# Optimization experiments

Hardware: AMD Instinct MI355X
Metric: run time of the kernel (lower is better)

The kernel has to match this reference:

```python
import jax, jax.numpy as jnp
import numpy as np

B, T, I, H, C, S, V = 32, 64, 300, 168, 168, 512, 50257


def setup_inputs() -> dict:
    key = jax.random.key(0)
    ks = jax.random.split(key, 10)
    s = 0.05
    return {
        "x": jax.random.normal(ks[0], (B, T, I), jnp.float32),
        "context": jax.random.normal(ks[1], (B, S, C), jnp.float32),
        "context_lengths": jax.random.randint(ks[2], (B,), 1, S + 1),
        "W_ih": jax.random.normal(ks[3], (4 * H, I + C), jnp.float32) * s,
        "W_hh": jax.random.normal(ks[4], (4 * H, H), jnp.float32) * s,
        "b_ih": jnp.zeros((4 * H,), jnp.float32),
        "b_hh": jnp.zeros((4 * H,), jnp.float32),
        "att_Wx": jax.random.normal(ks[5], (H, H), jnp.float32) * s,
        "att_Ws": jax.random.normal(ks[6], (C, H), jnp.float32) * s,
        "att_b": jnp.zeros((H,), jnp.float32),
        "att_v": jax.random.normal(ks[7], (H,), jnp.float32) * s,
        "W_dec": jax.random.normal(ks[8], (V, H), jnp.float32) * s,
    }


def reference(x, context, context_lengths, W_ih, W_hh, b_ih, b_hh,
              att_Wx, att_Ws, att_b, att_v, W_dec):
    # x: (B, T, I); context: (B, S, C)
    b, t, _ = x.shape
    s_len = context.shape[1]
    h_dim = W_hh.shape[1]
    dtype = x.dtype

    # valid-position mask for attention over source context
    mask = jnp.arange(s_len)[None, :] < context_lengths[:, None]  # (B, S)
    # seq projection is time-invariant: precompute once outside the step loop
    seq_proj = jnp.einsum('bsc,ca->bsa', context, att_Ws)  # (B, S, H)

    h0 = jnp.zeros((b, h_dim), dtype)
    c0 = jnp.zeros((b, h_dim), dtype)

    def step(carry, x_t):
        h, c = carry
        # MLP (additive) attention: v . tanh(Wx h + Ws seq + b)
        e = jnp.einsum('bsa,a->bs',
                       jnp.tanh((h @ att_Wx)[:, None, :] + seq_proj + att_b),
                       att_v)  # (B, S)
        e = jnp.where(mask, e, jnp.asarray(-1e9, dtype))
        w = jax.nn.softmax(e, axis=-1)
        attn_ctx = jnp.einsum('bs,bsc->bc', w, context)  # (B, C)

        # concat input with attended context, single-layer LSTM cell
        rnn_in = jnp.concatenate([x_t, attn_ctx], axis=1)  # (B, I+C)
        gates = rnn_in @ W_ih.T + b_ih + h @ W_hh.T + b_hh  # (B, 4H)
        i_g, f_g, g_g, o_g = jnp.split(gates, 4, axis=1)    # torch ifgo order
        c_new = jax.nn.sigmoid(f_g) * c + jax.nn.sigmoid(i_g) * jnp.tanh(g_g)
        h_new = jax.nn.sigmoid(o_g) * jnp.tanh(c_new)

        dec = h_new @ W_dec.T  # (B, V), bias-free decode
        return (h_new, c_new), dec

    _, decs = jax.lax.scan(step, (h0, c0), jnp.swapaxes(x, 0, 1))  # (T, B, V)
    return jnp.swapaxes(decs, 0, 1)  # (B, T, V)
```

## Files before the change

kernel.cpp:

```cpp
#include <hip/hip_runtime.h>
#include <stdint.h>

#define BB 32
#define TT 64
#define ID 300
#define HH 168
#define SS 512
#define VV 50257
#define G4 672
#define IC 468
#define KP 192
#define NP2 50432
#define NJ 8
#define RPB 21
#define CPB 84
#define KK 336
#define WKP 88
#define EPAD 170
#define SBLK 64
#define LSLOT 192
#define HROW 96
#define LP 72
#define NTN 197
#define NTILES 1576

typedef float f32x4 __attribute__((ext_vector_type(4)));
typedef short bf16x8 __attribute__((ext_vector_type(8)));
typedef unsigned long long u64;

__device__ __forceinline__ float bf2f(unsigned short u) {
  union { unsigned int i; float f; } v; v.i = ((unsigned int)u) << 16; return v.f;
}
__device__ __forceinline__ unsigned short f2bf(float f) {
  union { float f; unsigned int u; } v; v.f = f;
  unsigned int r = v.u + 0x7fffu + ((v.u >> 16) & 1u);
  return (unsigned short)(r >> 16);
}
__device__ __forceinline__ float rcpf(float x) { return __builtin_amdgcn_rcpf(x); }
__device__ __forceinline__ u64 packft(float f, unsigned tag) {
  union { float f; unsigned u; } v; v.f = f;
  return ((u64)tag << 32) | (u64)v.u;
}
__device__ __forceinline__ float lo_f(u64 x) {
  union { unsigned u; float f; } v; v.u = (unsigned)x; return v.f;
}
__device__ __forceinline__ unsigned hi_u(u64 x) { return (unsigned)(x >> 32); }
__device__ __forceinline__ void postv(u64* p, u64 v) {
  __hip_atomic_store(p, v, __ATOMIC_RELAXED, __HIP_MEMORY_SCOPE_AGENT);
}
__device__ __forceinline__ u64 loadv(const u64* p) {
  return __hip_atomic_load(p, __ATOMIC_RELAXED, __HIP_MEMORY_SCOPE_AGENT);
}
__device__ __forceinline__ void postu(unsigned* p, unsigned v) {
  __hip_atomic_store(p, v, __ATOMIC_RELAXED, __HIP_MEMORY_SCOPE_AGENT);
}
__device__ __forceinline__ unsigned loadu(const unsigned* p) {
  return __hip_atomic_load(p, __ATOMIC_RELAXED, __HIP_MEMORY_SCOPE_AGENT);
}

#define NB_WDEC 4728
#define NB_TR   788
__global__ void k_prepall(const float* __restrict__ Wih, const float* __restrict__ Whh,
                          const float* __restrict__ attWx, const float* __restrict__ Wd,
                          float* __restrict__ WihxT, unsigned short* __restrict__ Wdb,
                          float* __restrict__ WgT, unsigned short* __restrict__ WxS,
                          u64* __restrict__ Abuf, u64* __restrict__ Pbuf,
                          unsigned* __restrict__ pw) {
  const int bid = blockIdx.x, tid = threadIdx.x;
  if (bid < NB_WDEC) {
    size_t e0 = ((size_t)bid * 256 + tid) * 8;
    int v = (int)(e0 / KP), kp0 = (int)(e0 - (size_t)v * KP);
    int rg = kp0 / 24, off0 = kp0 - rg * 24;
    unsigned short o[8];
    if (v < VV) {
      const float* src = Wd + (size_t)v * HH + rg * RPB + off0;
      #pragma unroll
      for (int i = 0; i < 8; ++i) o[i] = (off0 + i < RPB) ? f2bf(src[i]) : 0;
    } else {
      #pragma unroll
      for (int i = 0; i < 8; ++i) o[i] = 0;
    }
    *(uint4*)(Wdb + e0) = *(const uint4*)o;
    return;
  }
  if (bid < NB_WDEC + NB_TR) {
    int idx = (bid - NB_WDEC) * 256 + tid;
    if (idx < ID * G4) {
      int k = idx / G4, i = idx - k * G4;
      WihxT[idx] = Wih[(size_t)i * IC + k];
    }
    return;
  }
  int idx = (bid - NB_WDEC - NB_TR) * 256 + tid;
  const int T1 = NJ * KK * WKP;
  const int T2 = T1 + NJ * RPB * HH;
  const int ZH = BB * NJ * LSLOT;
  const int T3 = T2 + 2 * ZH + 64;
  if (idx < T1) {
    int j = idx / (KK * WKP); int r = idx - j * (KK * WKP);
    int k = r / WKP, col = r - k * WKP;
    float w = 0.f;
    if (col < CPB) {
      int gt = col / RPB, rr = col - gt * RPB;
      int gcol = gt * HH + j * RPB + rr;
      w = (k < HH) ? Wih[(size_t)gcol * IC + ID + k] : Whh[(size_t)gcol * HH + (k - HH)];
    }
    WgT[idx] = w;
  } else if (idx < T2) {
    int r = idx - T1;
    WxS[r] = f2bf(attWx[r]);
  } else if (idx < T3) {
    int r = idx - T2;
    if (r < ZH) Abuf[r] = 0ull;
    else if (r < 2 * ZH) Pbuf[r - ZH] = 0ull;
    else pw[r - 2 * ZH] = 0u;
  }
}

__global__ void k_seqxp(const float* __restrict__ ctx, const float* __restrict__ Ws,
                        const float* __restrict__ x, const float* __restrict__ WihxT,
                        const float* __restrict__ bih, const float* __restrict__ bhh,
                        unsigned short* __restrict__ ETs, unsigned short* __restrict__ ctxb,
                        float* __restrict__ Xp) {
  __shared__ float sbuf[2688];
  const int tid = threadIdx.x;
  if (blockIdx.x < 1024) {
    const int b = blockIdx.x & 31;
    const int s0 = (blockIdx.x >> 5) * 16;
    for (int idx = tid; idx < 16 * HH; idx += 256) {
      float v = ctx[(size_t)(b * SS + s0) * HH + idx];
      sbuf[idx] = v;
      ctxb[(size_t)(b * SS + s0) * HH + idx] = f2bf(v);
    }
    __syncthreads();
    #pragma unroll
    for (int o = 0; o < 11; ++o) {
      int idx = o * 256 + tid;
      if (idx < 16 * HH) {
        int s = idx / HH, h = idx - s * HH;
        const float* cr = &sbuf[s * HH];
        float acc = 0.f;
        #pragma unroll 4
        for (int c = 0; c < HH; ++c) acc = fmaf(cr[c], Ws[c * HH + h], acc);
        ETs[(size_t)(b * SS + s0 + s) * HH + h] = f2bf(__expf(2.f * acc));
      }
    }
  } else {
    const int r = blockIdx.x - 1024;
    const int t0 = (r & 7) * 8;
    const int b = r >> 3;
    for (int idx = tid; idx < 8 * ID; idx += 256)
      sbuf[idx] = x[(size_t)(b * TT + t0) * ID + idx];
    __syncthreads();
    for (int i = tid; i < G4; i += 256) {
      float bias = bih[i] + bhh[i];
      float acc[8];
      #pragma unroll
      for (int tt = 0; tt < 8; ++tt) acc[tt] = bias;
      for (int k = 0; k < ID; ++k) {
        float w = WihxT[k * G4 + i];
        #pragma unroll
        for (int tt = 0; tt < 8; ++tt) acc[tt] += sbuf[tt * ID + k] * w;
      }
      #pragma unroll
      for (int tt = 0; tt < 8; ++tt)
        Xp[(size_t)(b * TT + t0 + tt) * G4 + i] = acc[tt];
    }
  }
}

__global__ __launch_bounds__(512, 1) void k_recur(
    const int* __restrict__ lens, const float* __restrict__ attb,
    const float* __restrict__ attv, const float* __restrict__ WgT,
    const unsigned short* __restrict__ WxS, const unsigned short* __restrict__ ETs,
    const unsigned short* __restrict__ ctxb, const float* __restrict__ Xp,
    u64* __restrict__ Abuf, u64* __restrict__ Pbuf,
    unsigned* __restrict__ hallA, const unsigned short* __restrict__ Wdb,
    float* __restrict__ out, unsigned* __restrict__ pw) {
  const int b = blockIdx.x & 31;
  const int j = blockIdx.x >> 5;
  const int tid = threadIdx.x;

  __shared__ __align__(16) float WgL[KK][WKP];
  __shared__ unsigned short EL[SBLK][EPAD];
  __shared__ unsigned short WxL[RPB][HH];
  __shared__ float scratch[512];
  __shared__ float redH[504], redC[504];
  __shared__ float gE[HH], hsh[HH], abL[HH], vL[HH], attn[HH];
  __shared__ float esh[SBLK], hLoc[RPB], cLoc[RPB], wsum[8];
  __shared__ float sumv_s, bsum_s;
  __shared__ int sClaim;

  {
    const f32x4* src = (const f32x4*)(WgT + (size_t)j * KK * WKP);
    f32x4* dst = (f32x4*)WgL;
    for (int i = tid; i < KK * WKP / 4; i += 512) dst[i] = src[i];
  }
  for (int i = tid; i < SBLK * HH; i += 512) {
    int s = i / HH, h = i - s * HH;
    EL[s][h] = ETs[((size_t)b * SS + j * SBLK + s) * HH + h];
  }
  for (int i = tid; i < RPB * HH; i += 512)
    ((unsigned short*)WxL)[i] = WxS[(size_t)j * RPB * HH + i];
  if (tid < HH) { abL[tid] = attb[tid]; vL[tid] = attv[tid]; }
  if (tid < RPB) cLoc[tid] = 0.f;
  __syncthreads();
  if (tid == 0) {
    float s = 0.f;
    for (int h = 0; h < HH; ++h) s += vL[h];
    sumv_s = s;
  }
  const int len = lens[b];
  const int sbase = j * SBLK;
  u64* Amine = Abuf + (size_t)(b * NJ + j) * LSLOT;
  u64* Pmine = Pbuf + (size_t)(b * NJ + j) * LSLOT;
  __syncthreads();

  for (int t = 0; t < TT; ++t) {
    float xa0=0,xa1=0,xa2=0,xa3=0, xb0=0,xb1=0,xb2=0,xb3=0;
    if (tid < 11) {
      const float* xp = Xp + ((size_t)b * TT + t) * G4 + j * RPB;
      int r0 = 2 * tid, r1 = r0 + 1;
      xa0 = xp[r0]; xa1 = xp[HH + r0]; xa2 = xp[2*HH + r0]; xa3 = xp[3*HH + r0];
      if (r1 < RPB) { xb0 = xp[r1]; xb1 = xp[HH + r1]; xb2 = xp[2*HH + r1]; xb3 = xp[3*HH + r1]; }
    }
    if (tid < HH) {
      float a = abL[tid], hv = 0.f;
      if (t > 0) {
        const unsigned want = (unsigned)t;
        const int jh = tid / RPB, hr = tid - jh * RPB;
        u64 va[9];
        int g = 0;
        for (;;) {
          #pragma unroll
          for (int jj = 0; jj < NJ; ++jj)
            va[jj] = loadv(&Abuf[(size_t)(b * NJ + jj) * LSLOT + tid]);
          va[8] = loadv(&Abuf[(size_t)(b * NJ + jh) * LSLOT + HH + hr]);
          bool ok = true;
          #pragma unroll
          for (int q = 0; q < 9; ++q) ok &= (hi_u(va[q]) >= want);
          if (ok) break;
          __builtin_amdgcn_s_sleep(1);
          if (++g > (1 << 24)) break;
        }
        #pragma unroll
        for (int jj = 0; jj < NJ; ++jj) a += lo_f(va[jj]);
        hv = lo_f(va[8]);
      }
      gE[tid] = __expf(2.f * a);
      hsh[tid] = hv;
    }
    __syncthreads();
    {
      int w = tid >> 6, lane = tid & 63;
      int sl = w * 8 + (lane >> 3);
      int hg = lane & 7;
      const unsigned short* er = &EL[sl][hg * RPB];
      const int hb = hg * RPB;
      float ep = 0.f;
      #pragma unroll 7
      for (int i = 0; i < RPB; ++i)
        ep += vL[hb + i] * rcpf(fmaf(gE[hb + i], bf2f(er[i]), 1.f));
      ep += __shfl_xor(ep, 1); ep += __shfl_xor(ep, 2); ep += __shfl_xor(ep, 4);
      float eh = (sbase + sl < len) ? __expf(sumv_s - 2.f * ep) : 0.f;
      float ws = (hg == 0) ? eh : 0.f;
      ws += __shfl_xor(ws, 8); ws += __shfl_xor(ws, 16); ws += __shfl_xor(ws, 32);
      if (lane == 0) wsum[w] = ws;
      if (hg == 0) esh[sl] = eh;
    }
    __syncthreads();
    if (tid < 504) {
      int c = tid % HH, ch = tid / HH;
      const unsigned short* cb = ctxb + ((size_t)b * SS + sbase) * HH + c;
      float p = 0.f;
      for (int s = ch; s < SBLK; s += 3)
        p = fmaf(esh[s], bf2f(cb[(size_t)s * HH]), p);
      scratch[ch * HH + c] = p;
    } else if (tid == 504) {
      float bs = 0.f;
      #pragma unroll
      for (int w = 0; w < 8; ++w) bs += wsum[w];
      bsum_s = bs;
    }
    __syncthreads();
    if (tid < HH) {
      float p = scratch[tid] + scratch[HH + tid] + scratch[2 * HH + tid];
      postv(&Pmine[tid], packft(p, (unsigned)(t + 1)));
    } else if (tid == HH) {
      postv(&Pmine[HH], packft(bsum_s, (unsigned)(t + 1)));
    }
    if (tid < 504) {
      int col = tid % CPB, kc = tid / CPB;
      int k0 = HH + kc * 28;
      float acc = 0.f;
      #pragma unroll 7
      for (int i = 0; i < 28; ++i)
        acc = fmaf(WgL[k0 + i][col], hsh[kc * 28 + i], acc);
      redH[kc * CPB + col] = acc;
    }
    if (tid < HH) {
      const unsigned want = (unsigned)(t + 1);
      u64 pv[NJ], bv[NJ];
      int g = 0;
      for (;;) {
        #pragma unroll
        for (int jj = 0; jj < NJ; ++jj) {
          const u64* pb = Pbuf + (size_t)(b * NJ + jj) * LSLOT;
          pv[jj] = loadv(&pb[tid]);
          bv[jj] = loadv(&pb[HH]);
        }
        bool ok = true;
        #pragma unroll
        for (int jj = 0; jj < NJ; ++jj) ok &= (hi_u(pv[jj]) >= want) & (hi_u(bv[jj]) >= want);
        if (ok) break;
        __builtin_amdgcn_s_sleep(1);
        if (++g > (1 << 24)) break;
      }
      float s = 0.f, den = 0.f;
      #pragma unroll
      for (int jj = 0; jj < NJ; ++jj) { s += lo_f(pv[jj]); den += lo_f(bv[jj]); }
      attn[tid] = s * rcpf(den);
    }
    __syncthreads();
    if (tid < 504) {
      int col = tid % CPB, kc = tid / CPB;
      int k0 = kc * 28;
      float acc = 0.f;
      #pragma unroll 7
      for (int i = 0; i < 28; ++i)
        acc = fmaf(WgL[k0 + i][col], attn[k0 + i], acc);
      redC[kc * CPB + col] = acc;
    }
    __syncthreads();
    if (tid < 12) {
      size_t hrow = ((size_t)b * TT + t) * HROW + j * 12;
      if (tid < 11) {
        const int r0 = 2 * tid, r1 = r0 + 1;
        float g0 = xa0, g1 = xa1, g2 = xa2, g3 = xa3;
        #pragma unroll
        for (int kc = 0; kc < 6; ++kc) {
          const float* rh = &redH[kc * CPB];
          const float* rc = &redC[kc * CPB];
          g0 += rh[r0] + rc[r0];
          g1 += rh[RPB + r0] + rc[RPB + r0];
          g2 += rh[2 * RPB + r0] + rc[2 * RPB + r0];
          g3 += rh[3 * RPB + r0] + rc[3 * RPB + r0];
        }
        float si = rcpf(1.f + __expf(-g0));
        float sf = rcpf(1.f + __expf(-g1));
        float tg = 1.f - 2.f * rcpf(1.f + __expf(2.f * g2));
        float so = rcpf(1.f + __expf(-g3));
        float cn = fmaf(sf, cLoc[r0], si * tg);
        float tc = 1.f - 2.f * rcpf(1.f + __expf(2.f * cn));
        float h0 = so * tc;
        cLoc[r0] = cn; hLoc[r0] = h0;
        unsigned hv = (unsigned)f2bf(h0);
        if (r1 < RPB) {
          float G0 = xb0, G1 = xb1, G2 = xb2, G3 = xb3;
          #pragma unroll
          for (int kc = 0; kc < 6; ++kc) {
            const float* rh = &redH[kc * CPB];
            const float* rc = &redC[kc * CPB];
            G0 += rh[r1] + rc[r1];
            G1 += rh[RPB + r1] + rc[RPB + r1];
            G2 += rh[2 * RPB + r1] + rc[2 * RPB + r1];
            G3 += rh[3 * RPB + r1] + rc[3 * RPB + r1];
          }
          float Si = rcpf(1.f + __expf(-G0));
          float Sf = rcpf(1.f + __expf(-G1));
          float Tg = 1.f - 2.f * rcpf(1.f + __expf(2.f * G2));
          float So = rcpf(1.f + __expf(-G3));
          float Cn = fmaf(Sf, cLoc[r1], Si * Tg);
          float Tc = 1.f - 2.f * rcpf(1.f + __expf(2.f * Cn));
          float h1 = So * Tc;
          cLoc[r1] = Cn; hLoc[r1] = h1;
          hv |= ((unsigned)f2bf(h1)) << 16;
        }
        postu(&hallA[hrow + tid], hv);
      } else {
        postu(&hallA[hrow + 11], 0u);
      }
    }
    __syncthreads();
    if (tid < HH) {
      float acc = 0.f;
      #pragma unroll
      for (int r = 0; r < RPB; ++r)
        acc = fmaf(hLoc[r], bf2f(WxL[r][tid]), acc);
      postv(&Amine[tid], packft(acc, (unsigned)(t + 1)));
    } else if (tid < HH + RPB) {
      postv(&Amine[tid], packft(hLoc[tid - HH], (unsigned)(t + 1)));
    }
  }

  __syncthreads();
  if (tid == 0) {
    __hip_atomic_fetch_add(&pw[0], 1u, __ATOMIC_RELAXED, __HIP_MEMORY_SCOPE_AGENT);
    int g = 0;
    while (loadu(&pw[0]) < (unsigned)(BB * NJ)) {
      __builtin_amdgcn_s_sleep(2);
      if (++g > (1 << 26)) break;
    }
  }
  __syncthreads();

  unsigned short* As = (unsigned short*)&WgL[0][0];
  unsigned short* Bs = As + 256 * LP;
  for (;;) {
    if (tid == 0) {
      unsigned w = __hip_atomic_fetch_add(&pw[32], 1u, __ATOMIC_RELAXED,
                                          __HIP_MEMORY_SCOPE_AGENT);
      sClaim = (w < NTILES) ? (int)w : -1;
    }
    __syncthreads();
    const int w = sClaim;
    if (w < 0) break;
    const int mt = w / NTN, nt = w - mt * NTN;
    const int m0 = mt * 256, n0 = nt * 256;
    const int lane = tid & 63, wid = tid >> 6;
    const int wm = wid >> 2, wn = wid & 3;
    const int lr = lane & 15, lk = lane >> 4;
    f32x4 acc[8][4];
    #pragma unroll
    for (int i = 0; i < 8; ++i)
      #pragma unroll
      for (int jj = 0; jj < 4; ++jj) acc[i][jj] = (f32x4)0.f;
    for (int k0 = 0; k0 < KP; k0 += 64) {
      if (k0) __syncthreads();
      #pragma unroll
      for (int i = 0; i < 4; ++i) {
        int flat = i * 512 + tid;
        int row = flat >> 3;
        int c8 = flat & 7;
        uint4 va = *(const uint4*)(hallA + (size_t)(m0 + row) * HROW + k0 / 2 + c8 * 4);
        *(uint4*)&As[row * LP + c8 * 8] = va;
        uint4 vb = *(const uint4*)(Wdb + (size_t)(n0 + row) * KP + k0 + c8 * 8);
        *(uint4*)&Bs[row * LP + c8 * 8] = vb;
      }
      __syncthreads();
      #pragma unroll
      for (int kk = 0; kk < 64; kk += 32) {
        bf16x8 af[8], bfr[4];
        #pragma unroll
        for (int mi = 0; mi < 8; ++mi)
          af[mi] = *(const bf16x8*)&As[(wm * 128 + mi * 16 + lr) * LP + kk + lk * 8];
        #pragma unroll
        for (int ni = 0; ni < 4; ++ni)
          bfr[ni] = *(const bf16x8*)&Bs[(wn * 64 + ni * 16 + lr) * LP + kk + lk * 8];
        #pragma unroll
        for (int mi = 0; mi < 8; ++mi)
          #pragma unroll
          for (int ni = 0; ni < 4; ++ni)
            acc[mi][ni] = __builtin_amdgcn_mfma_f32_16x16x32_bf16(
                af[mi], bfr[ni], acc[mi][ni], 0, 0, 0);
      }
    }
    #pragma unroll
    for (int mi = 0; mi < 8; ++mi)
      #pragma unroll
      for (int ni = 0; ni < 4; ++ni) {
        int col = n0 + wn * 64 + ni * 16 + lr;
        if (col < VV) {
          #pragma unroll
          for (int r = 0; r < 4; ++r) {
            int row = m0 + wm * 128 + mi * 16 + lk * 4 + r;
            out[(size_t)row * VV + col] = acc[mi][ni][r];
          }
        }
      }
    __syncthreads();
  }
}

extern "C" void kernel_launch(void* const* d_in, const int* in_sizes, int n_in,
                              void* d_out, int out_size, void* d_ws, size_t ws_size,
                              hipStream_t stream) {
  (void)in_sizes; (void)n_in; (void)out_size; (void)ws_size;
  const float* x     = (const float*)d_in[0];
  const float* ctx   = (const float*)d_in[1];
  const int*   lens  = (const int*)d_in[2];
  const float* Wih   = (const float*)d_in[3];
  const float* Whh   = (const float*)d_in[4];
  const float* bih   = (const float*)d_in[5];
  const float* bhh   = (const float*)d_in[6];
  const float* attWx = (const float*)d_in[7];
  const float* attWs = (const float*)d_in[8];
  const float* attb  = (const float*)d_in[9];
  const float* attv  = (const float*)d_in[10];
  const float* Wdec  = (const float*)d_in[11];
  float* out = (float*)d_out;

  char* base = (char*)d_ws;
  size_t off = 0;
  auto alloc = [&](size_t bytes) -> void* {
    off = (off + 255) & ~(size_t)255;
    void* p = base + off;
    off += bytes;
    return p;
  };
  unsigned short* ETs  = (unsigned short*)alloc((size_t)BB * SS * HH * 2);
  unsigned short* ctxb = (unsigned short*)alloc((size_t)BB * SS * HH * 2);
  float*          Xp   = (float*)alloc((size_t)BB * TT * G4 * 4);
  float*          WihxT= (float*)alloc((size_t)ID * G4 * 4);
  unsigned*       hallA= (unsigned*)alloc((size_t)BB * TT * HROW * 4);
  unsigned short* Wdb  = (unsigned short*)alloc((size_t)NP2 * KP * 2);
  float*          WgT  = (float*)alloc((size_t)NJ * KK * WKP * 4);
  unsigned short* WxS  = (unsigned short*)alloc((size_t)NJ * RPB * HH * 2);
  u64*            Abuf = (u64*)alloc((size_t)BB * NJ * LSLOT * 8);
  u64*            Pbuf = (u64*)alloc((size_t)BB * NJ * LSLOT * 8);
  unsigned*       pw   = (unsigned*)alloc(64 * 4);

  {
    const int TOTP = NJ * KK * WKP + NJ * RPB * HH + 2 * BB * NJ * LSLOT + 64;
    const int NBP = (TOTP + 255) / 256;
    k_prepall<<<dim3(NB_WDEC + NB_TR + NBP), dim3(256), 0, stream>>>(
        Wih, Whh, attWx, Wdec, WihxT, Wdb, WgT, WxS, Abuf, Pbuf, pw);
  }
  k_seqxp<<<dim3(1024 + 256), dim3(256), 0, stream>>>(ctx, attWs, x, WihxT,
                                                      bih, bhh, ETs, ctxb, Xp);
  {
    const int* a0 = lens; const float* a1 = attb; const float* a2 = attv;
    const float* a3 = WgT; const unsigned short* a4 = WxS;
    const unsigned short* a5 = ETs; const unsigned short* a6 = ctxb;
    const float* a7 = Xp; u64* a8 = Abuf; u64* a9 = Pbuf;
    unsigned* a10 = hallA; const unsigned short* a11 = Wdb;
    float* a12 = out; unsigned* a13 = pw;
    void* args[] = { &a0, &a1, &a2, &a3, &a4, &a5, &a6, &a7, &a8, &a9,
                     &a10, &a11, &a12, &a13 };
    hipLaunchCooperativeKernel((void*)k_recur, dim3(BB * NJ), dim3(512), args, 0, stream);
  }
}
```

Measured before the change: 834.2 us.

## Pair two batches per recurrence block and split decode GEMM into separate kernel

The recurrent cooperative kernel now runs half as many blocks, each handling two batch rows. The two rows' phases are interleaved so that one row's polling and compute can overlap the other's cross-block wait. The energy table is no longer staged in LDS; it is read from a padded global layout with vectorized loads. The vocabulary decode GEMM moves from a work-stealing tail inside the persistent kernel to a separate regular grid launch, which drops the global barrier and tile-claim atomics. The cost is longer serial per-step work per block and an extra kernel launch.

```diff
diff --git a/kernel.cpp b/kernel.cpp
--- a/kernel.cpp
+++ b/kernel.cpp
@@ -16,13 +16,12 @@
 #define CPB 84
 #define KK 336
 #define WKP 88
-#define EPAD 170
 #define SBLK 64
 #define LSLOT 192
 #define HROW 96
 #define LP 72
 #define NTN 197
-#define NTILES 1576
+#define EP 192
 
 typedef float f32x4 __attribute__((ext_vector_type(4)));
 typedef short bf16x8 __attribute__((ext_vector_type(8)));
@@ -53,9 +52,6 @@
 }
 __device__ __forceinline__ void postu(unsigned* p, unsigned v) {
   __hip_atomic_store(p, v, __ATOMIC_RELAXED, __HIP_MEMORY_SCOPE_AGENT);
-}
-__device__ __forceinline__ unsigned loadu(const unsigned* p) {
-  return __hip_atomic_load(p, __ATOMIC_RELAXED, __HIP_MEMORY_SCOPE_AGENT);
 }
 
 #define NB_WDEC 4728
@@ -64,8 +60,7 @@
                           const float* __restrict__ attWx, const float* __restrict__ Wd,
                           float* __restrict__ WihxT, unsigned short* __restrict__ Wdb,
                           float* __restrict__ WgT, unsigned short* __restrict__ WxS,
-                          u64* __restrict__ Abuf, u64* __restrict__ Pbuf,
-                          unsigned* __restrict__ pw) {
+                          u64* __restrict__ Abuf, u64* __restrict__ Pbuf) {
   const int bid = blockIdx.x, tid = threadIdx.x;
   if (bid < NB_WDEC) {
     size_t e0 = ((size_t)bid * 256 + tid) * 8;
@@ -95,7 +90,7 @@
   const int T1 = NJ * KK * WKP;
   const int T2 = T1 + NJ * RPB * HH;
   const int ZH = BB * NJ * LSLOT;
-  const int T3 = T2 + 2 * ZH + 64;
+  const int T3 = T2 + 2 * ZH;
   if (idx < T1) {
     int j = idx / (KK * WKP); int r = idx - j * (KK * WKP);
     int k = r / WKP, col = r - k * WKP;
@@ -112,15 +107,14 @@
   } else if (idx < T3) {
     int r = idx - T2;
     if (r < ZH) Abuf[r] = 0ull;
-    else if (r < 2 * ZH) Pbuf[r - ZH] = 0ull;
-    else pw[r - 2 * ZH] = 0u;
+    else        Pbuf[r - ZH] = 0ull;
   }
 }
 
 __global__ void k_seqxp(const float* __restrict__ ctx, const float* __restrict__ Ws,
                         const float* __restrict__ x, const float* __restrict__ WihxT,
                         const float* __restrict__ bih, const float* __restrict__ bhh,
-                        unsigned short* __restrict__ ETs, unsigned short* __restrict__ ctxb,
+                        unsigned short* __restrict__ ETsP, unsigned short* __restrict__ ctxb,
                         float* __restrict__ Xp) {
   __shared__ float sbuf[2688];
   const int tid = threadIdx.x;
@@ -142,7 +136,8 @@
         float acc = 0.f;
         #pragma unroll 4
         for (int c = 0; c < HH; ++c) acc = fmaf(cr[c], Ws[c * HH + h], acc);
-        ETs[(size_t)(b * SS + s0 + s) * HH + h] = f2bf(__expf(2.f * acc));
+        int hg = h / RPB, ho = h - hg * RPB;
+        ETsP[(size_t)(b * SS + s0 + s) * EP + hg * 24 + ho] = f2bf(__expf(2.f * acc));
       }
     }
   } else {
@@ -172,304 +167,339 @@
 __global__ __launch_bounds__(512, 1) void k_recur(
     const int* __restrict__ lens, const float* __restrict__ attb,
     const float* __restrict__ attv, const float* __restrict__ WgT,
-    const unsigned short* __restrict__ WxS, const unsigned short* __restrict__ ETs,
+    const unsigned short* __restrict__ WxS, const unsigned short* __restrict__ ETsP,
     const unsigned short* __restrict__ ctxb, const float* __restrict__ Xp,
     u64* __restrict__ Abuf, u64* __restrict__ Pbuf,
-    unsigned* __restrict__ hallA, const unsigned short* __restrict__ Wdb,
-    float* __restrict__ out, unsigned* __restrict__ pw) {
-  const int b = blockIdx.x & 31;
-  const int j = blockIdx.x >> 5;
+    unsigned* __restrict__ hallA) {
+  const int p = blockIdx.x & 15;
+  const int j = blockIdx.x >> 4;
+  const int b0 = 2 * p, b1 = 2 * p + 1;
   const int tid = threadIdx.x;
 
-  __shared__ __align__(16) float WgL[KK][WKP];
-  __shared__ unsigned short EL[SBLK][EPAD];
+  __shared__ float WgL[KK][WKP];
   __shared__ unsigned short WxL[RPB][HH];
   __shared__ float scratch[512];
-  __shared__ float redH[504], redC[504];
-  __shared__ float gE[HH], hsh[HH], abL[HH], vL[HH], attn[HH];
-  __shared__ float esh[SBLK], hLoc[RPB], cLoc[RPB], wsum[8];
-  __shared__ float sumv_s, bsum_s;
-  __shared__ int sClaim;
+  __shared__ float redH[2][504], redC[2][504];
+  __shared__ float gE[2][HH], hsh[2][HH], attn[2][HH];
+  __shared__ float abL[HH], vL[HH];
+  __shared__ float esh[2][SBLK], wsum[2][8];
+  __shared__ float hLoc[2][RPB], cLoc[2][RPB];
+  __shared__ float sumv_s, bsum_s[2];
 
   {
     const f32x4* src = (const f32x4*)(WgT + (size_t)j * KK * WKP);
     f32x4* dst = (f32x4*)WgL;
     for (int i = tid; i < KK * WKP / 4; i += 512) dst[i] = src[i];
   }
-  for (int i = tid; i < SBLK * HH; i += 512) {
-    int s = i / HH, h = i - s * HH;
-    EL[s][h] = ETs[((size_t)b * SS + j * SBLK + s) * HH + h];
-  }
   for (int i = tid; i < RPB * HH; i += 512)
     ((unsigned short*)WxL)[i] = WxS[(size_t)j * RPB * HH + i];
   if (tid < HH) { abL[tid] = attb[tid]; vL[tid] = attv[tid]; }
-  if (tid < RPB) cLoc[tid] = 0.f;
+  if (tid < RPB) { cLoc[0][tid] = 0.f; cLoc[1][tid] = 0.f; }
   __syncthreads();
   if (tid == 0) {
     float s = 0.f;
     for (int h = 0; h < HH; ++h) s += vL[h];
     sumv_s = s;
   }
-  const int len = lens[b];
+  const int len0 = lens[b0], len1 = lens[b1];
   const int sbase = j * SBLK;
-  u64* Amine = Abuf + (size_t)(b * NJ + j) * LSLOT;
-  u64* Pmine = Pbuf + (size_t)(b * NJ + j) * LSLOT;
+  u64* Am[2] = { Abuf + (size_t)(b0 * NJ + j) * LSLOT, Abuf + (size_t)(b1 * NJ + j) * LSLOT };
+  u64* Pm[2] = { Pbuf + (size_t)(b0 * NJ + j) * LSLOT, Pbuf + (size_t)(b1 * NJ + j) * LSLOT };
   __syncthreads();
 
   for (int t = 0; t < TT; ++t) {
-    float xa0=0,xa1=0,xa2=0,xa3=0, xb0=0,xb1=0,xb2=0,xb3=0;
+    float xa0[4] = {0,0,0,0}, xb0[4] = {0,0,0,0};
+    float xa1[4] = {0,0,0,0}, xb1[4] = {0,0,0,0};
     if (tid < 11) {
-      const float* xp = Xp + ((size_t)b * TT + t) * G4 + j * RPB;
+      const float* xp0 = Xp + ((size_t)b0 * TT + t) * G4 + j * RPB;
+      const float* xp1 = Xp + ((size_t)b1 * TT + t) * G4 + j * RPB;
       int r0 = 2 * tid, r1 = r0 + 1;
-      xa0 = xp[r0]; xa1 = xp[HH + r0]; xa2 = xp[2*HH + r0]; xa3 = xp[3*HH + r0];
-      if (r1 < RPB) { xb0 = xp[r1]; xb1 = xp[HH + r1]; xb2 = xp[2*HH + r1]; xb3 = xp[3*HH + r1]; }
-    }
-    if (tid < HH) {
-      float a = abL[tid], hv = 0.f;
-      if (t > 0) {
-        const unsigned want = (unsigned)t;
-        const int jh = tid / RPB, hr = tid - jh * RPB;
-        u64 va[9];
+      #pragma unroll
+      for (int q = 0; q < 4; ++q) xa0[q] = xp0[q * HH + r0];
+      #pragma unroll
+      for (int q = 0; q < 4; ++q) xa1[q] = xp1[q * HH + r0];
+      if (r1 < RPB) {
+        #pragma unroll
+        for (int q = 0; q < 4; ++q) xb0[q] = xp0[q * HH + r1];
+        #pragma unroll
+        for (int q = 0; q < 4; ++q) xb1[q] = xp1[q * HH + r1];
+      }
+    }
+
+    auto pollA = [&](int bb, int bi) {
+      if (tid < HH) {
+        float a = abL[tid], hv = 0.f;
+        if (t > 0) {
+          const unsigned want = (unsigned)t;
+          const int jh = tid / RPB, hr = tid - jh * RPB;
+          u64 va[9];
+          int g = 0;
+          for (;;) {
+            #pragma unroll
+            for (int jj = 0; jj < NJ; ++jj)
+              va[jj] = loadv(&Abuf[(size_t)(bb * NJ + jj) * LSLOT + tid]);
+            va[8] = loadv(&Abuf[(size_t)(bb * NJ + jh) * LSLOT + HH + hr]);
+            bool ok = true;
+            #pragma unroll
+            for (int q = 0; q < 9; ++q) ok &= (hi_u(va[q]) >= want);
+            if (ok) break;
+            __builtin_amdgcn_s_sleep(1);
+            if (++g > (1 << 24)) break;
+          }
+          #pragma unroll
+          for (int jj = 0; jj < NJ; ++jj) a += lo_f(va[jj]);
+          hv = lo_f(va[8]);
+        }
+        gE[bi][tid] = __expf(2.f * a);
+        hsh[bi][tid] = hv;
+      }
+    };
+    auto phaseB = [&](int bb, int bi, int lenb) {
+      int w = tid >> 6, lane = tid & 63;
+      int sl = w * 8 + (lane >> 3);
+      int hg = lane & 7;
+      const uint4* ep4 = (const uint4*)(ETsP + ((size_t)(bb * SS + sbase + sl) * EP + hg * 24));
+      union { uint4 q[3]; unsigned short s[24]; } eu;
+      eu.q[0] = ep4[0]; eu.q[1] = ep4[1]; eu.q[2] = ep4[2];
+      const int hb = hg * RPB;
+      float ep = 0.f;
+      #pragma unroll 7
+      for (int i = 0; i < RPB; ++i)
+        ep += vL[hb + i] * rcpf(fmaf(gE[bi][hb + i], bf2f(eu.s[i]), 1.f));
+      ep += __shfl_xor(ep, 1); ep += __shfl_xor(ep, 2); ep += __shfl_xor(ep, 4);
+      float eh = (sbase + sl < lenb) ? __expf(sumv_s - 2.f * ep) : 0.f;
+      float ws = (hg == 0) ? eh : 0.f;
+      ws += __shfl_xor(ws, 8); ws += __shfl_xor(ws, 16); ws += __shfl_xor(ws, 32);
+      if (lane == 0) wsum[bi][w] = ws;
+      if (hg == 0) esh[bi][sl] = eh;
+    };
+    auto phaseC = [&](int bb, int bi) {
+      if (tid < 504) {
+        int c = tid % HH, ch = tid / HH;
+        const unsigned short* cb = ctxb + ((size_t)bb * SS + sbase) * HH + c;
+        float pp = 0.f;
+        for (int s = ch; s < SBLK; s += 3)
+          pp = fmaf(esh[bi][s], bf2f(cb[(size_t)s * HH]), pp);
+        scratch[ch * HH + c] = pp;
+      } else if (tid == 504) {
+        float bs = 0.f;
+        #pragma unroll
+        for (int w = 0; w < 8; ++w) bs += wsum[bi][w];
+        bsum_s[bi] = bs;
+      }
+    };
+    auto postP = [&](int bi) {
+      if (tid < HH) {
+        float pp = scratch[tid] + scratch[HH + tid] + scratch[2 * HH + tid];
+        postv(&Pm[bi][tid], packft(pp, (unsigned)(t + 1)));
+      } else if (tid == HH) {
+        postv(&Pm[bi][HH], packft(bsum_s[bi], (unsigned)(t + 1)));
+      }
+    };
+    auto phaseDh = [&](int bi) {
+      if (tid < 504) {
+        int col = tid % CPB, kc = tid / CPB;
+        int k0 = HH + kc * 28;
+        float acc = 0.f;
+        #pragma unroll 7
+        for (int i = 0; i < 28; ++i)
+          acc = fmaf(WgL[k0 + i][col], hsh[bi][kc * 28 + i], acc);
+        redH[bi][kc * CPB + col] = acc;
+      }
+    };
+    auto pollP = [&](int bb, int bi, int base) {
+      int i = tid - base;
+      if (i >= 0 && i < HH) {
+        const unsigned want = (unsigned)(t + 1);
+        u64 pv[NJ], bv[NJ];
         int g = 0;
         for (;;) {
           #pragma unroll
-          for (int jj = 0; jj < NJ; ++jj)
-            va[jj] = loadv(&Abuf[(size_t)(b * NJ + jj) * LSLOT + tid]);
-          va[8] = loadv(&Abuf[(size_t)(b * NJ + jh) * LSLOT + HH + hr]);
+          for (int jj = 0; jj < NJ; ++jj) {
+            const u64* pb = Pbuf + (size_t)(bb * NJ + jj) * LSLOT;
+            pv[jj] = loadv(&pb[i]);
+            bv[jj] = loadv(&pb[HH]);
+          }
           bool ok = true;
           #pragma unroll
-          for (int q = 0; q < 9; ++q) ok &= (hi_u(va[q]) >= want);
+          for (int jj = 0; jj < NJ; ++jj) ok &= (hi_u(pv[jj]) >= want) & (hi_u(bv[jj]) >= want);
           if (ok) break;
           __builtin_amdgcn_s_sleep(1);
           if (++g > (1 << 24)) break;
         }
-        #pragma unroll
-        for (int jj = 0; jj < NJ; ++jj) a += lo_f(va[jj]);
-        hv = lo_f(va[8]);
-      }
-      gE[tid] = __expf(2.f * a);
-      hsh[tid] = hv;
-    }
-    __syncthreads();
-    {
-      int w = tid >> 6, lane = tid & 63;
-      int sl = w * 8 + (lane >> 3);
-      int hg = lane & 7;
-      const unsigned short* er = &EL[sl][hg * RPB];
-      const int hb = hg * RPB;
-      float ep = 0.f;
-      #pragma unroll 7
-      for (int i = 0; i < RPB; ++i)
-        ep += vL[hb + i] * rcpf(fmaf(gE[hb + i], bf2f(er[i]), 1.f));
-      ep += __shfl_xor(ep, 1); ep += __shfl_xor(ep, 2); ep += __shfl_xor(ep, 4);
-      float eh = (sbase + sl < len) ? __expf(sumv_s - 2.f * ep) : 0.f;
-      float ws = (hg == 0) ? eh : 0.f;
-      ws += __shfl_xor(ws, 8); ws += __shfl_xor(ws, 16); ws += __shfl_xor(ws, 32);
-      if (lane == 0) wsum[w] = ws;
-      if (hg == 0) esh[sl] = eh;
-    }
-    __syncthreads();
-    if (tid < 504) {
-      int c = tid % HH, ch = tid / HH;
-      const unsigned short* cb = ctxb + ((size_t)b * SS + sbase) * HH + c;
-      float p = 0.f;
-      for (int s = ch; s < SBLK; s += 3)
-        p = fmaf(esh[s], bf2f(cb[(size_t)s * HH]), p);
-      scratch[ch * HH + c] = p;
-    } else if (tid == 504) {
-      float bs = 0.f;
-      #pragma unroll
-      for (int w = 0; w < 8; ++w) bs += wsum[w];
-      bsum_s = bs;
-    }
-    __syncthreads();
-    if (tid < HH) {
-      float p = scratch[tid] + scratch[HH + tid] + scratch[2 * HH + tid];
-      postv(&Pmine[tid], packft(p, (unsigned)(t + 1)));
-    } else if (tid == HH) {
-      postv(&Pmine[HH], packft(bsum_s, (unsigned)(t + 1)));
-    }
-    if (tid < 504) {
-      int col = tid % CPB, kc = tid / CPB;
-      int k0 = HH + kc * 28;
-      float acc = 0.f;
-      #pragma unroll 7
-      for (int i = 0; i < 28; ++i)
-        acc = fmaf(WgL[k0 + i][col], hsh[kc * 28 + i], acc);
-      redH[kc * CPB + col] = acc;
-    }
-    if (tid < HH) {
-      const unsigned want = (unsigned)(t + 1);
-      u64 pv[NJ], bv[NJ];
-      int g = 0;
-      for (;;) {
-        #pragma unroll
-        for (int jj = 0; jj < NJ; ++jj) {
-          const u64* pb = Pbuf + (size_t)(b * NJ + jj) * LSLOT;
-          pv[jj] = loadv(&pb[tid]);
-          bv[jj] = loadv(&pb[HH]);
-        }
-        bool ok = true;
-        #pragma unroll
-        for (int jj = 0; jj < NJ; ++jj) ok &= (hi_u(pv[jj]) >= want) & (hi_u(bv[jj]) >= want);
-        if (ok) break;
-        __builtin_amdgcn_s_sleep(1);
-        if (++g > (1 << 24)) break;
-      }
-      float s = 0.f, den = 0.f;
-      #pragma unroll
-      for (int jj = 0; jj < NJ; ++jj) { s += lo_f(pv[jj]); den += lo_f(bv[jj]); }
-      attn[tid] = s * rcpf(den);
-    }
-    __syncthreads();
-    if (tid < 504) {
-      int col = tid % CPB, kc = tid / CPB;
-      int k0 = kc * 28;
-      float acc = 0.f;
-      #pragma unroll 7
-      for (int i = 0; i < 28; ++i)
-        acc = fmaf(WgL[k0 + i][col], attn[k0 + i], acc);
-      redC[kc * CPB + col] = acc;
-    }
-    __syncthreads();
-    if (tid < 12) {
-      size_t hrow = ((size_t)b * TT + t) * HROW + j * 12;
-      if (tid < 11) {
-        const int r0 = 2 * tid, r1 = r0 + 1;
-        float g0 = xa0, g1 = xa1, g2 = xa2, g3 = xa3;
-        #pragma unroll
-        for (int kc = 0; kc < 6; ++kc) {
-          const float* rh = &redH[kc * CPB];
-          const float* rc = &redC[kc * CPB];
-          g0 += rh[r0] + rc[r0];
-          g1 += rh[RPB + r0] + rc[RPB + r0];
-          g2 += rh[2 * RPB + r0] + rc[2 * RPB + r0];
-          g3 += rh[3 * RPB + r0] + rc[3 * RPB + r0];
-        }
-        float si = rcpf(1.f + __expf(-g0));
-        float sf = rcpf(1.f + __expf(-g1));
-        float tg = 1.f - 2.f * rcpf(1.f + __expf(2.f * g2));
-        float so = rcpf(1.f + __expf(-g3));
-        float cn = fmaf(sf, cLoc[r0], si * tg);
-        float tc = 1.f - 2.f * rcpf(1.f + __expf(2.f * cn));
-        float h0 = so * tc;
-        cLoc[r0] = cn; hLoc[r0] = h0;
-        unsigned hv = (unsigned)f2bf(h0);
-        if (r1 < RPB) {
-          float G0 = xb0, G1 = xb1, G2 = xb2, G3 = xb3;
+        float s = 0.f, den = 0.f;
+        #pragma unroll
+        for (int jj = 0; jj < NJ; ++jj) { s += lo_f(pv[jj]); den += lo_f(bv[jj]); }
+        attn[bi][i] = s * rcpf(den);
+      }
+    };
+    auto phaseDc = [&](int bi) {
+      if (tid < 504) {
+        int col = tid % CPB, kc = tid / CPB;
+        int k0 = kc * 28;
+        float acc = 0.f;
+        #pragma unroll 7
+        for (int i = 0; i < 28; ++i)
+          acc = fmaf(WgL[k0 + i][col], attn[bi][k0 + i], acc);
+        redC[bi][kc * CPB + col] = acc;
+      }
+    };
+    auto lstm = [&](int bb, int bi, const float* xa, const float* xb) {
+      if (tid < 12) {
+        size_t hrow = ((size_t)bb * TT + t) * HROW + j * 12;
+        if (tid < 11) {
+          const int r0 = 2 * tid, r1 = r0 + 1;
+          float g0 = xa[0], g1 = xa[1], g2 = xa[2], g3 = xa[3];
           #pragma unroll
           for (int kc = 0; kc < 6; ++kc) {
-            const float* rh = &redH[kc * CPB];
-            const float* rc = &redC[kc * CPB];
-            G0 += rh[r1] + rc[r1];
-            G1 += rh[RPB + r1] + rc[RPB + r1];
-            G2 += rh[2 * RPB + r1] + rc[2 * RPB + r1];
-            G3 += rh[3 * RPB + r1] + rc[3 * RPB + r1];
+            const float* rh = &redH[bi][kc * CPB];
+            const float* rc = &redC[bi][kc * CPB];
+            g0 += rh[r0] + rc[r0];
+            g1 += rh[RPB + r0] + rc[RPB + r0];
+            g2 += rh[2 * RPB + r0] + rc[2 * RPB + r0];
+            g3 += rh[3 * RPB + r0] + rc[3 * RPB + r0];
           }
-          float Si = rcpf(1.f + __expf(-G0));
-          float Sf = rcpf(1.f + __expf(-G1));
-          float Tg = 1.f - 2.f * rcpf(1.f + __expf(2.f * G2));
-          float So = rcpf(1.f + __expf(-G3));
-          float Cn = fmaf(Sf, cLoc[r1], Si * Tg);
-          float Tc = 1.f - 2.f * rcpf(1.f + __expf(2.f * Cn));
-          float h1 = So * Tc;
-          cLoc[r1] = Cn; hLoc[r1] = h1;
-          hv |= ((unsigned)f2bf(h1)) << 16;
+          float si = rcpf(1.f + __expf(-g0));
+          float sf = rcpf(1.f + __expf(-g1));
+          float tg = 1.f - 2.f * rcpf(1.f + __expf(2.f * g2));
+          float so = rcpf(1.f + __expf(-g3));
+          float cn = fmaf(sf, cLoc[bi][r0], si * tg);
+          float tc = 1.f - 2.f * rcpf(1.f + __expf(2.f * cn));
+          float h0 = so * tc;
+          cLoc[bi][r0] = cn; hLoc[bi][r0] = h0;
+          unsigned hv = (unsigned)f2bf(h0);
+          if (r1 < RPB) {
+            float G0 = xb[0], G1 = xb[1], G2 = xb[2], G3 = xb[3];
+            #pragma unroll
+            for (int kc = 0; kc < 6; ++kc) {
+              const float* rh = &redH[bi][kc * CPB];
+              const float* rc = &redC[bi][kc * CPB];
+              G0 += rh[r1] + rc[r1];
+              G1 += rh[RPB + r1] + rc[RPB + r1];
+              G2 += rh[2 * RPB + r1] + rc[2 * RPB + r1];
+              G3 += rh[3 * RPB + r1] + rc[3 * RPB + r1];
+            }
+            float Si = rcpf(1.f + __expf(-G0));
+            float Sf = rcpf(1.f + __expf(-G1));
+            float Tg = 1.f - 2.f * rcpf(1.f + __expf(2.f * G2));
+            float So = rcpf(1.f + __expf(-G3));
+            float Cn = fmaf(Sf, cLoc[bi][r1], Si * Tg);
+            float Tc = 1.f - 2.f * rcpf(1.f + __expf(2.f * Cn));
+            float h1 = So * Tc;
+            cLoc[bi][r1] = Cn; hLoc[bi][r1] = h1;
+            hv |= ((unsigned)f2bf(h1)) << 16;
+          }
+          postu(&hallA[hrow + tid], hv);
+        } else {
+          postu(&hallA[hrow + 11], 0u);
         }
-        postu(&hallA[hrow + tid], hv);
-      } else {
-        postu(&hallA[hrow + 11], 0u);
-      }
-    }
-    __syncthreads();
-    if (tid < HH) {
-      float acc = 0.f;
-      #pragma unroll
-      for (int r = 0; r < RPB; ++r)
-        acc = fmaf(hLoc[r], bf2f(WxL[r][tid]), acc);
-      postv(&Amine[tid], packft(acc, (unsigned)(t + 1)));
-    } else if (tid < HH + RPB) {
-      postv(&Amine[tid], packft(hLoc[tid - HH], (unsigned)(t + 1)));
-    }
-  }
-
-  __syncthreads();
-  if (tid == 0) {
-    __hip_atomic_fetch_add(&pw[0], 1u, __ATOMIC_RELAXED, __HIP_MEMORY_SCOPE_AGENT);
-    int g = 0;
-    while (loadu(&pw[0]) < (unsigned)(BB * NJ)) {
-      __builtin_amdgcn_s_sleep(2);
-      if (++g > (1 << 26)) break;
-    }
-  }
-  __syncthreads();
-
-  unsigned short* As = (unsigned short*)&WgL[0][0];
-  unsigned short* Bs = As + 256 * LP;
-  for (;;) {
-    if (tid == 0) {
-      unsigned w = __hip_atomic_fetch_add(&pw[32], 1u, __ATOMIC_RELAXED,
-                                          __HIP_MEMORY_SCOPE_AGENT);
-      sClaim = (w < NTILES) ? (int)w : -1;
-    }
-    __syncthreads();
-    const int w = sClaim;
-    if (w < 0) break;
-    const int mt = w / NTN, nt = w - mt * NTN;
-    const int m0 = mt * 256, n0 = nt * 256;
-    const int lane = tid & 63, wid = tid >> 6;
-    const int wm = wid >> 2, wn = wid & 3;
-    const int lr = lane & 15, lk = lane >> 4;
-    f32x4 acc[8][4];
+      }
+    };
+    auto aGemv = [&](int bi) {
+      if (tid < HH) {
+        float acc = 0.f;
+        #pragma unroll
+        for (int r = 0; r < RPB; ++r)
+          acc = fmaf(hLoc[bi][r], bf2f(WxL[r][tid]), acc);
+        postv(&Am[bi][tid], packft(acc, (unsigned)(t + 1)));
+      } else if (tid < HH + RPB) {
+        postv(&Am[bi][tid], packft(hLoc[bi][tid - HH], (unsigned)(t + 1)));
+      }
+    };
+
+    pollA(b0, 0);
+    __syncthreads();
+    phaseB(b0, 0, len0);
+    __syncthreads();
+    phaseC(b0, 0);
+    __syncthreads();
+    postP(0);
+    phaseDh(0);
+    pollA(b1, 1);
+    __syncthreads();
+    phaseB(b1, 1, len1);
+    __syncthreads();
+    phaseC(b1, 1);
+    __syncthreads();
+    postP(1);
+    phaseDh(1);
+    pollP(b0, 0, 0);
+    __syncthreads();
+    phaseDc(0);
+    __syncthreads();
+    lstm(b0, 0, xa0, xb0);
+    __syncthreads();
+    aGemv(0);
+    pollP(b1, 1, 256);
+    __syncthreads();
+    phaseDc(1);
+    __syncthreads();
+    lstm(b1, 1, xa1, xb1);
+    __syncthreads();
+    aGemv(1);
+  }
+}
+
+__global__ __launch_bounds__(512) void k_decode(const unsigned* __restrict__ hallA,
+                                                const unsigned short* __restrict__ wdb,
+                                                float* __restrict__ out) {
+  __shared__ __align__(16) unsigned short As[256 * LP];
+  __shared__ __align__(16) unsigned short Bs[256 * LP];
+  const unsigned short* hallS = (const unsigned short*)hallA;
+  const int tid = threadIdx.x;
+  const int n0 = blockIdx.x * 256, m0 = blockIdx.y * 256;
+  const int lane = tid & 63, wid = tid >> 6;
+  const int wm = wid >> 2, wn = wid & 3;
+  const int lr = lane & 15, lk = lane >> 4;
+  f32x4 acc[8][4];
+  #pragma unroll
+  for (int i = 0; i < 8; ++i)
     #pragma unroll
-    for (int i = 0; i < 8; ++i)
-      #pragma unroll
-      for (int jj = 0; jj < 4; ++jj) acc[i][jj] = (f32x4)0.f;
-    for (int k0 = 0; k0 < KP; k0 += 64) {
-      if (k0) __syncthreads();
-      #pragma unroll
-      for (int i = 0; i < 4; ++i) {
-        int flat = i * 512 + tid;
-        int row = flat >> 3;
-        int c8 = flat & 7;
-        uint4 va = *(const uint4*)(hallA + (size_t)(m0 + row) * HROW + k0 / 2 + c8 * 4);
-        *(uint4*)&As[row * LP + c8 * 8] = va;
-        uint4 vb = *(const uint4*)(Wdb + (size_t)(n0 + row) * KP + k0 + c8 * 8);
-        *(uint4*)&Bs[row * LP + c8 * 8] = vb;
-      }
-      __syncthreads();
-      #pragma unroll
-      for (int kk = 0; kk < 64; kk += 32) {
-        bf16x8 af[8], bfr[4];
-        #pragma unroll
-        for (int mi = 0; mi < 8; ++mi)
-          af[mi] = *(const bf16x8*)&As[(wm * 128 + mi * 16 + lr) * LP + kk + lk * 8];
+    for (int jj = 0; jj < 4; ++jj) acc[i][jj] = (f32x4)0.f;
+
+  for (int k0 = 0; k0 < KP; k0 += 64) {
+    if (k0) __syncthreads();
+    #pragma unroll
+    for (int i = 0; i < 4; ++i) {
+      int flat = i * 512 + tid;
+      int row = flat >> 3;
+      int c8 = flat & 7;
+      uint4 va = *(const uint4*)(hallS + (size_t)(m0 + row) * KP + k0 + c8 * 8);
+      *(uint4*)&As[row * LP + c8 * 8] = va;
+      uint4 vb = *(const uint4*)(wdb + (size_t)(n0 + row) * KP + k0 + c8 * 8);
+      *(uint4*)&Bs[row * LP + c8 * 8] = vb;
+    }
+    __syncthreads();
+    #pragma unroll
+    for (int kk = 0; kk < 64; kk += 32) {
+      bf16x8 af[8], bfr[4];
+      #pragma unroll
+      for (int mi = 0; mi < 8; ++mi)
+        af[mi] = *(const bf16x8*)&As[(wm * 128 + mi * 16 + lr) * LP + kk + lk * 8];
+      #pragma unroll
+      for (int ni = 0; ni < 4; ++ni)
+        bfr[ni] = *(const bf16x8*)&Bs[(wn * 64 + ni * 16 + lr) * LP + kk + lk * 8];
+      #pragma unroll
+      for (int mi = 0; mi < 8; ++mi)
         #pragma unroll
         for (int ni = 0; ni < 4; ++ni)
-          bfr[ni] = *(const bf16x8*)&Bs[(wn * 64 + ni * 16 + lr) * LP + kk + lk * 8];
-        #pragma unroll
-        for (int mi = 0; mi < 8; ++mi)
-          #pragma unroll
-          for (int ni = 0; ni < 4; ++ni)
-            acc[mi][ni] = __builtin_amdgcn_mfma_f32_16x16x32_bf16(
-                af[mi], bfr[ni], acc[mi][ni], 0, 0, 0);
-      }
-    }
+          acc[mi][ni] = __builtin_amdgcn_mfma_f32_16x16x32_bf16(
+              af[mi], bfr[ni], acc[mi][ni], 0, 0, 0);
+    }
+  }
+  #pragma unroll
+  for (int mi = 0; mi < 8; ++mi)
     #pragma unroll
-    for (int mi = 0; mi < 8; ++mi)
-      #pragma unroll
-      for (int ni = 0; ni < 4; ++ni) {
-        int col = n0 + wn * 64 + ni * 16 + lr;
-        if (col < VV) {
-          #pragma unroll
-          for (int r = 0; r < 4; ++r) {
-            int row = m0 + wm * 128 + mi * 16 + lk * 4 + r;
-            out[(size_t)row * VV + col] = acc[mi][ni][r];
-          }
+    for (int ni = 0; ni < 4; ++ni) {
+      int col = n0 + wn * 64 + ni * 16 + lr;
+      if (col < VV) {
+        #pragma unroll
+        for (int r = 0; r < 4; ++r) {
+          int row = m0 + wm * 128 + mi * 16 + lk * 4 + r;
+          out[(size_t)row * VV + col] = acc[mi][ni][r];
         }
       }
-    __syncthreads();
-  }
+    }
 }
 
 extern "C" void kernel_launch(void* const* d_in, const int* in_sizes, int n_in,
@@ -498,7 +528,7 @@
     off += bytes;
     return p;
   };
-  unsigned short* ETs  = (unsigned short*)alloc((size_t)BB * SS * HH * 2);
+  unsigned short* ETsP = (unsigned short*)alloc((size_t)BB * SS * EP * 2);
   unsigned short* ctxb = (unsigned short*)alloc((size_t)BB * SS * HH * 2);
   float*          Xp   = (float*)alloc((size_t)BB * TT * G4 * 4);
   float*          WihxT= (float*)alloc((size_t)ID * G4 * 4);
@@ -508,25 +538,23 @@
   unsigned short* WxS  = (unsigned short*)alloc((size_t)NJ * RPB * HH * 2);
   u64*            Abuf = (u64*)alloc((size_t)BB * NJ * LSLOT * 8);
   u64*            Pbuf = (u64*)alloc((size_t)BB * NJ * LSLOT * 8);
-  unsigned*       pw   = (unsigned*)alloc(64 * 4);
 
   {
-    const int TOTP = NJ * KK * WKP + NJ * RPB * HH + 2 * BB * NJ * LSLOT + 64;
+    const int TOTP = NJ * KK * WKP + NJ * RPB * HH + 2 * BB * NJ * LSLOT;
     const int NBP = (TOTP + 255) / 256;
     k_prepall<<<dim3(NB_WDEC + NB_TR + NBP), dim3(256), 0, stream>>>(
-        Wih, Whh, attWx, Wdec, WihxT, Wdb, WgT, WxS, Abuf, Pbuf, pw);
+        Wih, Whh, attWx, Wdec, WihxT, Wdb, WgT, WxS, Abuf, Pbuf);
   }
   k_seqxp<<<dim3(1024 + 256), dim3(256), 0, stream>>>(ctx, attWs, x, WihxT,
-                                                      bih, bhh, ETs, ctxb, Xp);
+                                                      bih, bhh, ETsP, ctxb, Xp);
   {
     const int* a0 = lens; const float* a1 = attb; const float* a2 = attv;
     const float* a3 = WgT; const unsigned short* a4 = WxS;
-    const unsigned short* a5 = ETs; const unsigned short* a6 = ctxb;
+    const unsigned short* a5 = ETsP; const unsigned short* a6 = ctxb;
     const float* a7 = Xp; u64* a8 = Abuf; u64* a9 = Pbuf;
-    unsigned* a10 = hallA; const unsigned short* a11 = Wdb;
-    float* a12 = out; unsigned* a13 = pw;
-    void* args[] = { &a0, &a1, &a2, &a3, &a4, &a5, &a6, &a7, &a8, &a9,
-                     &a10, &a11, &a12, &a13 };
-    hipLaunchCooperativeKernel((void*)k_recur, dim3(BB * NJ), dim3(512), args, 0, stream);
-  }
-}
+    unsigned* a10 = hallA;
+    void* args[] = { &a0, &a1, &a2, &a3, &a4, &a5, &a6, &a7, &a8, &a9, &a10 };
+    hipLaunchCooperativeKernel((void*)k_recur, dim3(BB * NJ / 2), dim3(512), args, 0, stream);
+  }
+  k_decode<<<dim3(NTN, 8), dim3(512), 0, stream>>>(hallA, Wdb, out);
+}
```

After: 1.328 ms. +59.1%, slower.
